# Optimization experiments

Hardware: AMD Instinct MI355X
Metric: run time of the kernel (lower is better)

## Reference

```python
import jax, jax.numpy as jnp
import numpy as np

NEG_SLOPE = 0.2  # PyG GATv2Conv default negative_slope


def gatv2_conv(x, src, dst, Wl, bl, Wr, br, att, bias, concat=True):
    # x: [N, Fin]; src/dst: [E] (message flows src -> dst, softmax over dst)
    N = x.shape[0]
    H, C = att.shape
    xl = (x @ Wl + bl).reshape(N, H, C)  # source-side transform (lin_l)
    xr = (x @ Wr + br).reshape(N, H, C)  # target-side transform (lin_r)
    e = xl[src] + xr[dst]                              # [E, H, C]
    score = jnp.sum(jax.nn.leaky_relu(e, NEG_SLOPE) * att, axis=-1)  # [E, H]
    # segment softmax over incoming edges of each target node
    m = jax.ops.segment_max(score, dst, num_segments=N)               # [N, H]
    a = jnp.exp(score - m[dst])
    denom = jax.ops.segment_sum(a, dst, num_segments=N)               # [N, H]
    alpha = a / denom[dst]                                            # [E, H]
    out = jax.ops.segment_sum(xl[src] * alpha[..., None], dst, num_segments=N)  # [N, H, C]
    if concat:
        out = out.reshape(N, H * C)
    else:
        out = out.mean(axis=1)
    return out + bias


def setup_inputs() -> dict:
    key = jax.random.key(0)
    ks = jax.random.split(key, 12)
    N, E, Fin = 100000, 1600000, 128
    H1, C1 = 8, 16
    C2 = 64
    def glorot(k, shape):
        fan_in, fan_out = shape[0], shape[-1]
        lim = (6.0 / (fan_in + fan_out)) ** 0.5
        return jax.random.uniform(k, shape, jnp.float32, -lim, lim)
    x = jax.random.normal(ks[0], (N, Fin), jnp.float32)
    edge_index = jax.random.randint(ks[1], (2, E), 0, N, dtype=jnp.int64)
    return {
        "x": x,
        "edge_index": edge_index,
        "Wl1": glorot(ks[2], (Fin, H1 * C1)),
        "bl1": jnp.zeros((H1 * C1,), jnp.float32),
        "Wr1": glorot(ks[3], (Fin, H1 * C1)),
        "br1": jnp.zeros((H1 * C1,), jnp.float32),
        "att1": glorot(ks[4], (H1, C1)),
        "bias1": jnp.zeros((H1 * C1,), jnp.float32),
        "Wl2": glorot(ks[5], (H1 * C1, C2)),
        "bl2": jnp.zeros((C2,), jnp.float32),
        "Wr2": glorot(ks[6], (H1 * C1, C2)),
        "br2": jnp.zeros((C2,), jnp.float32),
        "att2": glorot(ks[7], (1, C2)),
        "bias2": jnp.zeros((C2,), jnp.float32),
    }


def reference(x, edge_index, Wl1, bl1, Wr1, br1, att1, bias1,
              Wl2, bl2, Wr2, br2, att2, bias2):
    N = x.shape[0]
    loops = jnp.arange(N, dtype=edge_index.dtype)
    src = jnp.concatenate([edge_index[0], loops])  # PyG adds self loops by default
    dst = jnp.concatenate([edge_index[1], loops])
    # eval mode: F.dropout(training=False) is identity
    h = gatv2_conv(x, src, dst, Wl1, bl1, Wr1, br1, att1, bias1, concat=True)
    h = jax.nn.elu(h)
    out = gatv2_conv(h, src, dst, Wl2, bl2, Wr2, br2, att2, bias2, concat=True)
    return out
```

## Files before the change

### kernel.cpp

```cpp
#include <hip/hip_runtime.h>
#include <math.h>

#define FIN 128
#define F1  128
#define C2  64
#define NEG 0.2f

#define BKT_SHIFT 8
#define BKT_SIZE  256
#define BKT_CAP   5120
#define SCAT_CHUNK 4096
#define IMGCAP 8192

typedef _Float16 half4 __attribute__((ext_vector_type(4)));
typedef _Float16 f16x8 __attribute__((ext_vector_type(8)));
typedef _Float16 h2    __attribute__((ext_vector_type(2)));
typedef float    f32x4 __attribute__((ext_vector_type(4)));

union H8u { f16x8 v; h2 p[4]; };

#if __has_builtin(__builtin_amdgcn_fdot2)
__device__ __forceinline__ float fdot2_acc(h2 a, h2 b, float c) {
  return __builtin_amdgcn_fdot2(a, b, c, false);
}
#else
__device__ __forceinline__ float fdot2_acc(h2 a, h2 b, float c) {
  return c + (float)a[0] * (float)b[0] + (float)a[1] * (float)b[1];
}
#endif

__global__ __launch_bounds__(256) void bucket_scatter_kernel(
    const int* __restrict__ ei, int* __restrict__ bcur, int* __restrict__ tmp,
    int E, int ET, int NBKT) {
  __shared__ int sh_hist[512];
  __shared__ int sh_pref[512];
  __shared__ int sh_gbase[512];
  __shared__ int img[SCAT_CHUNK];
  __shared__ unsigned short bkt[SCAT_CHUNK];
  __shared__ int sh_tot;
  const int t = threadIdx.x;
  for (int b = t; b < NBKT; b += 256) sh_hist[b] = 0;
  if (t == 0) sh_tot = 0;
  __syncthreads();
  const int g0 = blockIdx.x * SCAT_CHUNK + t;
  int bk[16], pk[16];
#pragma unroll
  for (int i = 0; i < 16; ++i) {
    const int g = g0 + i * 256;
    int b = -1, p = 0;
    if (g < ET) {
      const int src = (g < E) ? ei[g] : (g - E);
      const int dst = (g < E) ? ei[E + g] : (g - E);
      b = dst >> BKT_SHIFT;
      p = (src << BKT_SHIFT) | (dst & (BKT_SIZE - 1));
      atomicAdd(&sh_hist[b], 1);
    }
    bk[i] = b; pk[i] = p;
  }
  __syncthreads();
  for (int b = t; b < NBKT; b += 256) {
    const int c = sh_hist[b];
    if (c) {
      sh_pref[b]  = atomicAdd(&sh_tot, c);
      sh_gbase[b] = b * BKT_CAP + atomicAdd(&bcur[b], c);
    }
    sh_hist[b] = 0;
  }
  __syncthreads();
#pragma unroll
  for (int i = 0; i < 16; ++i) {
    if (bk[i] >= 0) {
      const int slot = sh_pref[bk[i]] + atomicAdd(&sh_hist[bk[i]], 1);
      img[slot] = pk[i];
      bkt[slot] = (unsigned short)bk[i];
    }
  }
  __syncthreads();
  const int tot = sh_tot;
  for (int j = t; j < tot; j += 256) {
    const int b = bkt[j];
    tmp[sh_gbase[b] + (j - sh_pref[b])] = img[j];
  }
}

__global__ __launch_bounds__(256) void build_csr_kernel(
    const int* __restrict__ tmp, const int* __restrict__ bcnt,
    int2* __restrict__ ind2, int* __restrict__ csr, int N) {
  __shared__ int cnt[256];
  __shared__ int cur[256];
  __shared__ int img[IMGCAP];
  const int b = blockIdx.x;
  const int t = threadIdx.x;
  const int base = b * BKT_CAP;
  const int cntb = bcnt[b];
  cnt[t] = 0;
  __syncthreads();
  for (int i = t; i < cntb; i += 256)
    atomicAdd(&cnt[tmp[base + i] & (BKT_SIZE - 1)], 1);
  __syncthreads();
  const int v = cnt[t];
  cur[t] = v;
  __syncthreads();
  for (int off = 1; off < 256; off <<= 1) {
    int val = (t >= off) ? cur[t - off] : 0;
    __syncthreads();
    cur[t] += val;
    __syncthreads();
  }
  const int excl = cur[t] - v;
  const int node = (b << BKT_SHIFT) + t;
  if (node < N) ind2[node] = make_int2(base + excl, base + excl + v);
  __syncthreads();
  cur[t] = excl;
  __syncthreads();
  if (cntb <= IMGCAP) {
    for (int i = t; i < cntb; i += 256) {
      const int p = tmp[base + i];
      const int pos = atomicAdd(&cur[p & (BKT_SIZE - 1)], 1);
      img[pos] = p >> BKT_SHIFT;
    }
    __syncthreads();
    for (int i = t; i < cntb; i += 256) csr[base + i] = img[i];
  } else {
    for (int i = t; i < cntb; i += 256) {
      const int p = tmp[base + i];
      const int pos = atomicAdd(&cur[p & (BKT_SIZE - 1)], 1);
      csr[base + pos] = p >> BKT_SHIFT;
    }
  }
}

__global__ __launch_bounds__(256) void wtrans_kernel(
    const float* __restrict__ W0, const float* __restrict__ W1,
    const float* __restrict__ W2, const float* __restrict__ W3,
    _Float16* __restrict__ T0, _Float16* __restrict__ T1,
    _Float16* __restrict__ T2, _Float16* __restrict__ T3) {
  const int m = blockIdx.y;
  const float* W = (m == 0) ? W0 : (m == 1) ? W1 : (m == 2) ? W2 : W3;
  _Float16* T = (m == 0) ? T0 : (m == 1) ? T1 : (m == 2) ? T2 : T3;
  const int ncols = (m < 2) ? 128 : 64;
  const int idx = blockIdx.x * 256 + threadIdx.x;
  if (idx < ncols * 128) {
    const int n = idx >> 7;
    const int k = idx & 127;
    T[idx] = (_Float16)W[k * ncols + n];
  }
}

template<int NCOLS, int CPW, bool AF32>
__global__ __launch_bounds__(256) void gemm_dual_kernel(
    const void* __restrict__ Av,
    const _Float16* __restrict__ WtL, const float* __restrict__ bLp, _Float16* __restrict__ OL,
    const _Float16* __restrict__ WtR, const float* __restrict__ bRp, _Float16* __restrict__ ORp,
    int M) {
  __shared__ _Float16 lds[16 * 136];
  const int tid  = threadIdx.x;
  const int wave = tid >> 6;
  const int lane = tid & 63;
  const int row16 = lane & 15;
  const int quad  = lane >> 4;
  const int kb = quad * 8;
  f16x8 bfL[CPW][4], bfR[CPW][4];
  float bvL[CPW], bvR[CPW];
#pragma unroll
  for (int c = 0; c < CPW; ++c) {
    const int n0 = (wave * CPW + c) * 16;
    bvL[c] = bLp[n0 + row16];
    bvR[c] = bRp[n0 + row16];
#pragma unroll
    for (int kt = 0; kt < 4; ++kt) {
      bfL[c][kt] = *(const f16x8*)(WtL + (n0 + row16) * 128 + kt * 32 + kb);
      bfR[c][kt] = *(const f16x8*)(WtR + (n0 + row16) * 128 + kt * 32 + kb);
    }
  }
  const int rowTiles = (M + 15) >> 4;
  for (int rt = blockIdx.x; rt < rowTiles; rt += gridDim.x) {
    const int r0 = rt << 4;
    if constexpr (AF32) {
      const float4* x4 = (const float4*)Av;
#pragma unroll
      for (int i = 0; i < 2; ++i) {
        const int fi = i * 256 + tid;
        const int gr = fi >> 5;
        const int gc = fi & 31;
        const int row = min(r0 + gr, M - 1);
        const float4 u = x4[(size_t)row * 32 + gc];
        half4 h;
        h.x = (_Float16)u.x; h.y = (_Float16)u.y;
        h.z = (_Float16)u.z; h.w = (_Float16)u.w;
        *(half4*)(lds + gr * 136 + gc * 4) = h;
      }
    } else {
      const _Float16* A = (const _Float16*)Av;
      const int gr = tid >> 4;
      const int gc = tid & 15;
      const int row = min(r0 + gr, M - 1);
      *(f16x8*)(lds + gr * 136 + gc * 8) = *(const f16x8*)(A + (size_t)row * 128 + gc * 8);
    }
    __syncthreads();
    f16x8 af[4];
#pragma unroll
    for (int kt = 0; kt < 4; ++kt)
      af[kt] = *(const f16x8*)(lds + row16 * 136 + kt * 32 + kb);
    f32x4 accL[CPW], accR[CPW];
#pragma unroll
    for (int c = 0; c < CPW; ++c) {
      accL[c] = (f32x4){0.f, 0.f, 0.f, 0.f};
      accR[c] = (f32x4){0.f, 0.f, 0.f, 0.f};
    }
#pragma unroll
    for (int kt = 0; kt < 4; ++kt) {
#pragma unroll
      for (int c = 0; c < CPW; ++c) {
        accL[c] = __builtin_amdgcn_mfma_f32_16x16x32_f16(af[kt], bfL[c][kt], accL[c], 0, 0, 0);
        accR[c] = __builtin_amdgcn_mfma_f32_16x16x32_f16(af[kt], bfR[c][kt], accR[c], 0, 0, 0);
      }
    }
#pragma unroll
    for (int c = 0; c < CPW; ++c) {
      const int col = (wave * CPW + c) * 16 + row16;
#pragma unroll
      for (int r = 0; r < 4; ++r) {
        const int row = r0 + quad * 4 + r;
        if (row < M) {
          OL[(size_t)row * NCOLS + col]  = (_Float16)(accL[c][r] + bvL[c]);
          ORp[(size_t)row * NCOLS + col] = (_Float16)(accR[c][r] + bvR[c]);
        }
      }
    }
    __syncthreads();
  }
}

template<int LSH, int XORS, int B>
__device__ __forceinline__ void attn_block(const _Float16* __restrict__ xlp,
                                           const int* __restrict__ csr, int e,
                                           const H8u& xru, const H8u& atu,
                                           float& l, float (&acc)[8]) {
  const h2 neg2 = {(_Float16)NEG, (_Float16)NEG};
  int s[B];
#pragma unroll
  for (int i = 0; i < B; ++i) s[i] = csr[e + i];
  H8u x[B];
#pragma unroll
  for (int i = 0; i < B; ++i) x[i].v = *(const f16x8*)(xlp + ((size_t)s[i] << LSH));
  float t[B];
#pragma unroll
  for (int i = 0; i < B; ++i) {
    float tv = 0.f;
#pragma unroll
    for (int j = 0; j < 4; ++j) {
      h2 ev = x[i].p[j] + xru.p[j];
      ev = __builtin_elementwise_max(ev, ev * neg2);
      tv = fdot2_acc(ev, atu.p[j], tv);
    }
    t[i] = tv;
  }
#pragma unroll
  for (int i = 0; i < B; ++i) {
    t[i] += __shfl_xor(t[i], 1);
    if constexpr (XORS >= 2) t[i] += __shfl_xor(t[i], 2);
    if constexpr (XORS >= 3) t[i] += __shfl_xor(t[i], 4);
  }
  float p[B];
#pragma unroll
  for (int i = 0; i < B; ++i) { p[i] = __expf(t[i]); l += p[i]; }
#pragma unroll
  for (int i = 0; i < B; ++i) {
#pragma unroll
    for (int j = 0; j < 4; ++j) {
      acc[2*j]   = fmaf(p[i], (float)x[i].p[j][0], acc[2*j]);
      acc[2*j+1] = fmaf(p[i], (float)x[i].p[j][1], acc[2*j+1]);
    }
  }
}

template<int LSH, int XORS>
__device__ __forceinline__ void attn_edges(const _Float16* __restrict__ xlp,
                                           const int* __restrict__ csr,
                                           int beg, int end,
                                           const H8u& xru, const H8u& atu,
                                           float& l, float (&acc)[8]) {
  int e = beg;
  for (; e + 4 <= end; e += 4) attn_block<LSH, XORS, 4>(xlp, csr, e, xru, atu, l, acc);
  if (e + 2 <= end) { attn_block<LSH, XORS, 2>(xlp, csr, e, xru, atu, l, acc); e += 2; }
  if (e < end)      { attn_block<LSH, XORS, 1>(xlp, csr, e, xru, atu, l, acc); }
}

__global__ __launch_bounds__(256) void attn1_kernel(
    const _Float16* __restrict__ xl, const _Float16* __restrict__ xr,
    const float* __restrict__ att, const float* __restrict__ bias,
    const int2* __restrict__ ind2, const int* __restrict__ csr,
    _Float16* __restrict__ hout, int N) {
  const int lane = threadIdx.x & 15;
  const int v = blockIdx.x * 16 + (threadIdx.x >> 4);
  if (v >= N) return;
  const int c8 = lane << 3;
  const _Float16* xlp = xl + c8;
  H8u xru; xru.v = *(const f16x8*)(xr + ((size_t)v << 7) + c8);
  H8u atu;
  {
    const float4 a0 = *(const float4*)(att + c8);
    const float4 a1 = *(const float4*)(att + c8 + 4);
    f16x8 a;
    a[0] = (_Float16)a0.x; a[1] = (_Float16)a0.y; a[2] = (_Float16)a0.z; a[3] = (_Float16)a0.w;
    a[4] = (_Float16)a1.x; a[5] = (_Float16)a1.y; a[6] = (_Float16)a1.z; a[7] = (_Float16)a1.w;
    atu.v = a;
  }
  const int2 be = ind2[v];
  const int beg = be.x;
  const int end = be.y;
  float l = 0.f;
  float acc[8] = {0.f, 0.f, 0.f, 0.f, 0.f, 0.f, 0.f, 0.f};
  attn_edges<7, 1>(xlp, csr, beg, end, xru, atu, l, acc);

  const float rl = 1.f / l;
  const float4 bb0 = *(const float4*)(bias + c8);
  const float4 bb1 = *(const float4*)(bias + c8 + 4);
  float r[8];
  r[0] = fmaf(acc[0], rl, bb0.x); r[1] = fmaf(acc[1], rl, bb0.y);
  r[2] = fmaf(acc[2], rl, bb0.z); r[3] = fmaf(acc[3], rl, bb0.w);
  r[4] = fmaf(acc[4], rl, bb1.x); r[5] = fmaf(acc[5], rl, bb1.y);
  r[6] = fmaf(acc[6], rl, bb1.z); r[7] = fmaf(acc[7], rl, bb1.w);
  f16x8 hres;
#pragma unroll
  for (int i = 0; i < 8; ++i) {
    const float z = r[i] > 0.f ? r[i] : expm1f(r[i]);
    hres[i] = (_Float16)z;
  }
  *(f16x8*)(hout + ((size_t)v << 7) + c8) = hres;
}

__global__ __launch_bounds__(256) void attn2_kernel(
    const _Float16* __restrict__ xl, const _Float16* __restrict__ xr,
    const float* __restrict__ att, const float* __restrict__ bias,
    const int2* __restrict__ ind2, const int* __restrict__ csr,
    float* __restrict__ out, int N) {
  const int lane = threadIdx.x & 7;
  const int v = blockIdx.x * 32 + (threadIdx.x >> 3);
  if (v >= N) return;
  const int c8 = lane << 3;
  const _Float16* xlp = xl + c8;
  H8u xru; xru.v = *(const f16x8*)(xr + ((size_t)v << 6) + c8);
  H8u atu;
  {
    const float4 a0 = *(const float4*)(att + c8);
    const float4 a1 = *(const float4*)(att + c8 + 4);
    f16x8 a;
    a[0] = (_Float16)a0.x; a[1] = (_Float16)a0.y; a[2] = (_Float16)a0.z; a[3] = (_Float16)a0.w;
    a[4] = (_Float16)a1.x; a[5] = (_Float16)a1.y; a[6] = (_Float16)a1.z; a[7] = (_Float16)a1.w;
    atu.v = a;
  }
  const int2 be = ind2[v];
  const int beg = be.x;
  const int end = be.y;
  float l = 0.f;
  float acc[8] = {0.f, 0.f, 0.f, 0.f, 0.f, 0.f, 0.f, 0.f};
  attn_edges<6, 3>(xlp, csr, beg, end, xru, atu, l, acc);

  const float rl = 1.f / l;
  const float4 bb0 = *(const float4*)(bias + c8);
  const float4 bb1 = *(const float4*)(bias + c8 + 4);
  float4 o0, o1;
  o0.x = fmaf(acc[0], rl, bb0.x); o0.y = fmaf(acc[1], rl, bb0.y);
  o0.z = fmaf(acc[2], rl, bb0.z); o0.w = fmaf(acc[3], rl, bb0.w);
  o1.x = fmaf(acc[4], rl, bb1.x); o1.y = fmaf(acc[5], rl, bb1.y);
  o1.z = fmaf(acc[6], rl, bb1.z); o1.w = fmaf(acc[7], rl, bb1.w);
  *(float4*)(out + ((size_t)v << 6) + c8) = o0;
  *(float4*)(out + ((size_t)v << 6) + c8 + 4) = o1;
}

extern "C" void kernel_launch(void* const* d_in, const int* in_sizes, int n_in,
                              void* d_out, int out_size, void* d_ws, size_t ws_size,
                              hipStream_t stream) {
  const float* x     = (const float*)d_in[0];
  const int*   ei    = (const int*)d_in[1];
  const float* Wl1   = (const float*)d_in[2];
  const float* bl1   = (const float*)d_in[3];
  const float* Wr1   = (const float*)d_in[4];
  const float* br1   = (const float*)d_in[5];
  const float* att1  = (const float*)d_in[6];
  const float* bias1 = (const float*)d_in[7];
  const float* Wl2   = (const float*)d_in[8];
  const float* bl2   = (const float*)d_in[9];
  const float* Wr2   = (const float*)d_in[10];
  const float* br2   = (const float*)d_in[11];
  const float* att2  = (const float*)d_in[12];
  const float* bias2 = (const float*)d_in[13];

  const int N  = in_sizes[0] / FIN;
  const int E  = in_sizes[1] / 2;
  const int ET = E + N;
  const int NBKT = (N + BKT_SIZE - 1) >> BKT_SHIFT;

  _Float16* xl1h  = (_Float16*)d_ws;
  _Float16* xr1h  = xl1h + (size_t)N * F1;
  _Float16* hbufh = xr1h + (size_t)N * F1;
  _Float16* Wt1l  = hbufh + (size_t)N * F1;
  _Float16* Wt1r  = Wt1l + 128 * 128;
  _Float16* Wt2l  = Wt1r + 128 * 128;
  _Float16* Wt2r  = Wt2l + 64 * 128;
  int2* ind2  = (int2*)(Wt2r + 64 * 128);
  int* csr    = (int*)(ind2 + N);
  int* bcur   = csr + (size_t)NBKT * BKT_CAP;
  int* tmp    = (int*)hbufh;
  _Float16* xl2h = xl1h;
  _Float16* xr2h = xr1h;
  float* out  = (float*)d_out;

  const int sblocks = (ET + SCAT_CHUNK - 1) / SCAT_CHUNK;

  hipMemsetAsync(bcur, 0, 512 * sizeof(int), stream);
  bucket_scatter_kernel<<<sblocks, 256, 0, stream>>>(ei, bcur, tmp, E, ET, NBKT);
  build_csr_kernel<<<NBKT, 256, 0, stream>>>(tmp, bcur, ind2, csr, N);

  wtrans_kernel<<<dim3(64, 4), 256, 0, stream>>>(Wl1, Wr1, Wl2, Wr2, Wt1l, Wt1r, Wt2l, Wt2r);

  gemm_dual_kernel<128, 2, true><<<1024, 256, 0, stream>>>(
      x, Wt1l, bl1, xl1h, Wt1r, br1, xr1h, N);

  attn1_kernel<<<(N + 15) / 16, 256, 0, stream>>>(xl1h, xr1h, att1, bias1, ind2, csr, hbufh, N);

  gemm_dual_kernel<64, 1, false><<<1024, 256, 0, stream>>>(
      hbufh, Wt2l, bl2, xl2h, Wt2r, br2, xr2h, N);

  attn2_kernel<<<(N + 31) / 32, 256, 0, stream>>>(xl2h, xr2h, att2, bias2, ind2, csr, out, N);
}
```

Before: 294.5 us.

## Fuse layer-2 dual GEMM into layer-1 attention epilogue via LDS and MFMA

The layer-1 attention kernel now keeps each block's 16 ELU outputs in shared memory. It then runs the layer-2 left and right projections directly with 16x16x32 f16 MFMA instructions. This removes the hidden-activation write and re-read through global memory and drops one kernel launch. The layer-2 outputs are moved into the freed h region. The grid is now N/16 with the bounds check removed, so it assumes N is a multiple of 16, which holds for N=100000. Each block also reloads the Wt2 weights from global memory.

```diff
diff --git a/kernel.cpp b/kernel.cpp
--- a/kernel.cpp
+++ b/kernel.cpp
@@ -287,15 +287,19 @@
   if (e < end)      { attn_block<LSH, XORS, 1>(xlp, csr, e, xru, atu, l, acc); }
 }
 
-__global__ __launch_bounds__(256) void attn1_kernel(
+__global__ __launch_bounds__(256) void attn1_fused_kernel(
     const _Float16* __restrict__ xl, const _Float16* __restrict__ xr,
     const float* __restrict__ att, const float* __restrict__ bias,
     const int2* __restrict__ ind2, const int* __restrict__ csr,
-    _Float16* __restrict__ hout, int N) {
-  const int lane = threadIdx.x & 15;
-  const int v = blockIdx.x * 16 + (threadIdx.x >> 4);
-  if (v >= N) return;
-  const int c8 = lane << 3;
+    const _Float16* __restrict__ Wt2l, const float* __restrict__ bl2, _Float16* __restrict__ OL,
+    const _Float16* __restrict__ Wt2r, const float* __restrict__ br2, _Float16* __restrict__ ORp,
+    int N) {
+  __shared__ _Float16 hlds[16 * 136];
+  const int tid = threadIdx.x;
+  const int lane16 = tid & 15;
+  const int nodeLoc = tid >> 4;
+  const int v = blockIdx.x * 16 + nodeLoc;
+  const int c8 = lane16 << 3;
   const _Float16* xlp = xl + c8;
   H8u xru; xru.v = *(const f16x8*)(xr + ((size_t)v << 7) + c8);
   H8u atu;
@@ -308,11 +312,9 @@
     atu.v = a;
   }
   const int2 be = ind2[v];
-  const int beg = be.x;
-  const int end = be.y;
   float l = 0.f;
   float acc[8] = {0.f, 0.f, 0.f, 0.f, 0.f, 0.f, 0.f, 0.f};
-  attn_edges<7, 1>(xlp, csr, beg, end, xru, atu, l, acc);
+  attn_edges<7, 1>(xlp, csr, be.x, be.y, xru, atu, l, acc);
 
   const float rl = 1.f / l;
   const float4 bb0 = *(const float4*)(bias + c8);
@@ -328,7 +330,38 @@
     const float z = r[i] > 0.f ? r[i] : expm1f(r[i]);
     hres[i] = (_Float16)z;
   }
-  *(f16x8*)(hout + ((size_t)v << 7) + c8) = hres;
+  *(f16x8*)(hlds + nodeLoc * 136 + c8) = hres;
+  __syncthreads();
+
+  const int wave  = tid >> 6;
+  const int lane  = tid & 63;
+  const int row16 = lane & 15;
+  const int quad  = lane >> 4;
+  const int kb = quad * 8;
+  const int n0 = wave * 16 + row16;
+  const float bvL = bl2[n0];
+  const float bvR = br2[n0];
+  f16x8 af[4], bfL[4], bfR[4];
+#pragma unroll
+  for (int kt = 0; kt < 4; ++kt) {
+    af[kt]  = *(const f16x8*)(hlds + row16 * 136 + kt * 32 + kb);
+    bfL[kt] = *(const f16x8*)(Wt2l + n0 * 128 + kt * 32 + kb);
+    bfR[kt] = *(const f16x8*)(Wt2r + n0 * 128 + kt * 32 + kb);
+  }
+  f32x4 accL = (f32x4){0.f, 0.f, 0.f, 0.f};
+  f32x4 accR = (f32x4){0.f, 0.f, 0.f, 0.f};
+#pragma unroll
+  for (int kt = 0; kt < 4; ++kt) {
+    accL = __builtin_amdgcn_mfma_f32_16x16x32_f16(af[kt], bfL[kt], accL, 0, 0, 0);
+    accR = __builtin_amdgcn_mfma_f32_16x16x32_f16(af[kt], bfR[kt], accR, 0, 0, 0);
+  }
+  const int r0 = blockIdx.x * 16;
+#pragma unroll
+  for (int rr = 0; rr < 4; ++rr) {
+    const int row = r0 + quad * 4 + rr;
+    OL[(size_t)row * C2 + n0]  = (_Float16)(accL[rr] + bvL);
+    ORp[(size_t)row * C2 + n0] = (_Float16)(accR[rr] + bvR);
+  }
 }
 
 __global__ __launch_bounds__(256) void attn2_kernel(
@@ -395,17 +428,17 @@
 
   _Float16* xl1h  = (_Float16*)d_ws;
   _Float16* xr1h  = xl1h + (size_t)N * F1;
-  _Float16* hbufh = xr1h + (size_t)N * F1;
-  _Float16* Wt1l  = hbufh + (size_t)N * F1;
+  _Float16* hregion = xr1h + (size_t)N * F1;
+  _Float16* Wt1l  = hregion + (size_t)N * F1;
   _Float16* Wt1r  = Wt1l + 128 * 128;
   _Float16* Wt2l  = Wt1r + 128 * 128;
   _Float16* Wt2r  = Wt2l + 64 * 128;
   int2* ind2  = (int2*)(Wt2r + 64 * 128);
   int* csr    = (int*)(ind2 + N);
   int* bcur   = csr + (size_t)NBKT * BKT_CAP;
-  int* tmp    = (int*)hbufh;
-  _Float16* xl2h = xl1h;
-  _Float16* xr2h = xr1h;
+  int* tmp    = (int*)hregion;
+  _Float16* xl2h = hregion;
+  _Float16* xr2h = hregion + (size_t)N * C2;
   float* out  = (float*)d_out;
 
   const int sblocks = (ET + SCAT_CHUNK - 1) / SCAT_CHUNK;
@@ -419,10 +452,9 @@
   gemm_dual_kernel<128, 2, true><<<1024, 256, 0, stream>>>(
       x, Wt1l, bl1, xl1h, Wt1r, br1, xr1h, N);
 
-  attn1_kernel<<<(N + 15) / 16, 256, 0, stream>>>(xl1h, xr1h, att1, bias1, ind2, csr, hbufh, N);
-
-  gemm_dual_kernel<64, 1, false><<<1024, 256, 0, stream>>>(
-      hbufh, Wt2l, bl2, xl2h, Wt2r, br2, xr2h, N);
+  attn1_fused_kernel<<<N / 16, 256, 0, stream>>>(
+      xl1h, xr1h, att1, bias1, ind2, csr,
+      Wt2l, bl2, xl2h, Wt2r, br2, xr2h, N);
 
   attn2_kernel<<<(N + 31) / 32, 256, 0, stream>>>(xl2h, xr2h, att2, bias2, ind2, csr, out, N);
 }
```

Result: no change. 298.8 us (+1.5%).
